# Optimization experiments

Hardware: AMD Instinct MI355X
Metric: run time of the kernel (lower is better)

## Reference

```python
import jax, jax.numpy as jnp
import numpy as np

B, T, I, H, O = 64, 2048, 128, 256, 128
K1 = 1
K2 = 1


def setup_inputs() -> dict:
    key = jax.random.key(0)
    ks = jax.random.split(key, 8)
    M = H - K1 + 1
    return {
        "x": jax.random.normal(ks[0], (B, T, I), jnp.float32),
        "W_in": jax.random.normal(ks[1], (H, I), jnp.float32) / np.sqrt(I).astype(np.float32),
        "b_in": jax.random.normal(ks[2], (H,), jnp.float32) * 0.01,
        "W_out": jax.random.normal(ks[3], (O, H), jnp.float32) / np.sqrt(H).astype(np.float32),
        "b_out": jax.random.normal(ks[4], (O,), jnp.float32) * 0.01,
        # padded Householder vectors: row i uses its first K+i entries (masked in reference)
        # uniform in [0.5, 1.5] keeps u.u well away from 0 (avoids 2/<u,u> blowup)
        "u_raw": jax.random.uniform(ks[5], (M, H), jnp.float32, 0.5, 1.5),
        "sigmas": jnp.ones((H,), jnp.float32),
        "v_raw": jax.random.uniform(ks[6], (M, H), jnp.float32, 0.5, 1.5),
    }


def _householder_chain(hats):
    # U <- H_last @ ... @ H_0, H_i = I - 2/<u,u> u u^T, applied as rank-1 updates
    Hdim = hats.shape[1]
    def step(Umat, u):
        beta = 2.0 / jnp.dot(u, u)
        return Umat - beta * jnp.outer(u, u @ Umat), None
    U, _ = jax.lax.scan(step, jnp.eye(Hdim, dtype=hats.dtype), hats)
    return U


def reference(x, W_in, b_in, W_out, b_out, u_raw, sigmas, v_raw):
    Hdim = sigmas.shape[0]
    Mu = u_raw.shape[0]
    Mv = v_raw.shape[0]
    # row i of u_hats has entries in cols [0, K1+i), then flipped along cols
    mask_u = jnp.arange(Hdim)[None, :] < (K1 + jnp.arange(Mu))[:, None]
    u_hats = jnp.flip(jnp.where(mask_u, u_raw, 0.0), axis=1)
    mask_v = jnp.arange(Hdim)[None, :] < (K2 + jnp.arange(Mv))[:, None]
    v_hats = jnp.flip(jnp.where(mask_v, v_raw, 0.0), axis=(0, 1))  # torch.flip dims=[0,1]
    U = _householder_chain(u_hats)
    V = _householder_chain(v_hats)
    W = (U * sigmas[None, :]) @ V  # U @ diag(sigmas) @ V
    # precompute input projection for all timesteps: [T, B, H]
    xproj = jnp.einsum('bti,hi->tbh', x, W_in) + b_in
    h0 = jnp.zeros((x.shape[0], Hdim), x.dtype)
    def cell(h, xp):
        h = jnp.tanh(xp + h @ W.T)
        return h, h @ W_out.T + b_out
    _, out = jax.lax.scan(cell, h0, xproj)  # out: [T, B, O]
    return jnp.transpose(out, (1, 0, 2))
```

## Files before the change

### kernel.cpp

```cpp
#include <hip/hip_runtime.h>
#include <hip/hip_bf16.h>
#include <hip/hip_fp16.h>

#define BB 64
#define TT 2048
#define II 128
#define HH 256
#define OO 128
#define RCH 8

typedef _Float16 f16x2 __attribute__((ext_vector_type(2)));
typedef _Float16 f16x8 __attribute__((ext_vector_type(8)));
typedef float f32x4 __attribute__((ext_vector_type(4)));

#if __has_builtin(__builtin_amdgcn_fdot2)
__device__ __forceinline__ float fdot2(f16x2 a, f16x2 b, float c) {
    return __builtin_amdgcn_fdot2(a, b, c, false);
}
#else
__device__ __forceinline__ float fdot2(f16x2 a, f16x2 b, float c) {
    return fmaf((float)a.x, (float)b.x, fmaf((float)a.y, (float)b.y, c));
}
#endif

__device__ __forceinline__ f16x2 u2h(unsigned int u) { return __builtin_bit_cast(f16x2, u); }
__device__ __forceinline__ unsigned int packf16(float a, float b) {
    return __builtin_bit_cast(unsigned int, f16x2{(_Float16)a, (_Float16)b});
}

__device__ __forceinline__ float tanh_fast(float x) {
    float xc = fminf(fmaxf(x, -9.0f), 9.0f);
    float e = __expf(2.0f * xc);
    return (e - 1.0f) * __fdividef(1.0f, e + 1.0f);
}

__global__ __launch_bounds__(64) void prep_kernel(
    const float* __restrict__ u_raw, const float* __restrict__ v_raw,
    float* __restrict__ u_eff, float* __restrict__ v_eff,
    float* __restrict__ beta_u, float* __restrict__ beta_v)
{
    const int row = blockIdx.x;
    const int lane = threadIdx.x;
    const bool isU = row < HH;
    const int i = isU ? row : row - HH;
    const float* src = isU ? (u_raw + (size_t)i * HH) : (v_raw + (size_t)(HH - 1 - i) * HH);
    float* dst = (isU ? u_eff : v_eff) + (size_t)i * HH;
    const int lo = isU ? (HH - 1 - i) : i;
    float ss = 0.0f;
    for (int c = lane; c < HH; c += 64) {
        float vv = (c >= lo) ? src[HH - 1 - c] : 0.0f;
        dst[c] = vv;
        ss += vv * vv;
    }
    for (int m = 1; m < 64; m <<= 1) ss += __shfl_xor(ss, m, 64);
    if (lane == 0) (isU ? beta_u : beta_v)[i] = 2.0f / ss;
}

__global__ __launch_bounds__(256) void hh_kernel(
    const float* __restrict__ u_eff, const float* __restrict__ v_eff,
    const float* __restrict__ beta_u, const float* __restrict__ beta_v,
    float* __restrict__ Ucol, float* __restrict__ Vrow)
{
    const int wid = blockIdx.x * 4 + (threadIdx.x >> 6);
    const int lane = threadIdx.x & 63;
    const bool isU = wid < HH;
    const int j = isU ? wid : wid - HH;
    const float* eff = isU ? u_eff : v_eff;
    const float* beta = isU ? beta_u : beta_v;

    float cr0 = (j == 4 * lane + 0) ? 1.0f : 0.0f;
    float cr1 = (j == 4 * lane + 1) ? 1.0f : 0.0f;
    float cr2 = (j == 4 * lane + 2) ? 1.0f : 0.0f;
    float cr3 = (j == 4 * lane + 3) ? 1.0f : 0.0f;

    const int i0 = isU ? (HH - 1 - j) : 0;
    for (int i = i0; i < HH; ++i) {
        const float4 v4 = *(const float4*)(eff + (size_t)i * HH + lane * 4);
        float d = v4.x * cr0 + v4.y * cr1 + v4.z * cr2 + v4.w * cr3;
        for (int m = 1; m < 64; m <<= 1) d += __shfl_xor(d, m, 64);
        const float t = beta[i] * d;
        cr0 = fmaf(-t, v4.x, cr0);
        cr1 = fmaf(-t, v4.y, cr1);
        cr2 = fmaf(-t, v4.z, cr2);
        cr3 = fmaf(-t, v4.w, cr3);
    }
    if (isU) {
        *(float4*)(Ucol + (size_t)j * HH + lane * 4) = make_float4(cr0, cr1, cr2, cr3);
    } else {
        Vrow[(size_t)(4 * lane + 0) * HH + j] = cr0;
        Vrow[(size_t)(4 * lane + 1) * HH + j] = cr1;
        Vrow[(size_t)(4 * lane + 2) * HH + j] = cr2;
        Vrow[(size_t)(4 * lane + 3) * HH + j] = cr3;
    }
}

__global__ __launch_bounds__(256) void w_kernel(
    const float* __restrict__ Ucol, const float* __restrict__ Vrow,
    const float* __restrict__ sig, float* __restrict__ Wm)
{
    const int r = blockIdx.x;
    const int c = threadIdx.x;
    float acc = 0.0f;
    #pragma unroll 4
    for (int k = 0; k < HH; ++k) {
        acc = fmaf(Ucol[(size_t)k * HH + r] * sig[k], Vrow[(size_t)k * HH + c], acc);
    }
    Wm[(size_t)r * HH + c] = acc;
}

__device__ __forceinline__ void stage16(_Float16* dst, const float* src) {
    #pragma unroll
    for (int i = 0; i < 4; ++i) {
        float4 f = ((const float4*)src)[i];
        ((f16x2*)dst)[2 * i + 0] = f16x2{(_Float16)f.x, (_Float16)f.y};
        ((f16x2*)dst)[2 * i + 1] = f16x2{(_Float16)f.z, (_Float16)f.w};
    }
}
__device__ __forceinline__ void stage16(_Float16* dst, const __half* src) {
    ((uint4*)dst)[0] = ((const uint4*)src)[0];
    ((uint4*)dst)[1] = ((const uint4*)src)[1];
}
__device__ __forceinline__ void storeC(float* p, float v) { *p = v; }
__device__ __forceinline__ void storeC(__half* p, float v) { *p = __float2half_rn(v); }

template <typename AT, typename OT>
__global__ __launch_bounds__(256) void gemm_mfma(
    const AT* __restrict__ A, const float* __restrict__ Bm,
    const float* __restrict__ bias, OT* __restrict__ C,
    int M, int N, int K)
{
    __shared__ _Float16 As[128][40];
    __shared__ _Float16 Bs[64][40];
    const int tid = threadIdx.x;
    const int m0 = blockIdx.x * 128;
    const int n0 = blockIdx.y * 64;
    const int lane = tid & 63;
    const int w = tid >> 6;
    const int lo = lane & 15;
    const int qd = lane >> 4;
    const int mh = w >> 1;
    const int nh = w & 1;
    const int srow = tid >> 1;
    const int shalf = tid & 1;

    f32x4 acc[4][2] = {};
    for (int k0 = 0; k0 < K; k0 += 32) {
        stage16(&As[srow][shalf * 16], A + (size_t)(m0 + srow) * K + k0 + shalf * 16);
        if (tid < 128)
            stage16(&Bs[srow][shalf * 16], Bm + (size_t)(n0 + srow) * K + k0 + shalf * 16);
        __syncthreads();
        f16x8 af[4], bf[2];
        #pragma unroll
        for (int mt = 0; mt < 4; ++mt)
            af[mt] = *(const f16x8*)&As[64 * mh + 16 * mt + lo][qd * 8];
        #pragma unroll
        for (int nt = 0; nt < 2; ++nt)
            bf[nt] = *(const f16x8*)&Bs[32 * nh + 16 * nt + lo][qd * 8];
        #pragma unroll
        for (int mt = 0; mt < 4; ++mt)
            #pragma unroll
            for (int nt = 0; nt < 2; ++nt)
                acc[mt][nt] = __builtin_amdgcn_mfma_f32_16x16x32_f16(
                    af[mt], bf[nt], acc[mt][nt], 0, 0, 0);
        __syncthreads();
    }
    #pragma unroll
    for (int nt = 0; nt < 2; ++nt) {
        const int n = n0 + 32 * nh + 16 * nt + lo;
        const float bv = bias[n];
        #pragma unroll
        for (int mt = 0; mt < 4; ++mt) {
            const int m = m0 + 64 * mh + 16 * mt + 4 * qd;
            #pragma unroll
            for (int r = 0; r < 4; ++r)
                storeC(C + (size_t)(m + r) * N + n, acc[mt][nt][r] + bv);
        }
    }
}

__global__ __launch_bounds__(512) void recur_kernel(
    const float* __restrict__ Wm,
    const __half* __restrict__ xp,
    __half* __restrict__ hall)
{
    const int b = blockIdx.x;
    const int tid = threadIdx.x;
    const int l = tid & 63;
    const int q = tid >> 6;

    __shared__ float ps[8][HH];
    __shared__ unsigned int hbits[2][HH / 2];

    f16x2 w2[4][16];
    #pragma unroll
    for (int r = 0; r < 4; ++r) {
        const float* Wp = Wm + (size_t)(4 * l + r) * HH + q * 32;
        #pragma unroll
        for (int c4 = 0; c4 < 8; ++c4) {
            float4 f = *(const float4*)(Wp + c4 * 4);
            w2[r][c4 * 2 + 0] = f16x2{(_Float16)f.x, (_Float16)f.y};
            w2[r][c4 * 2 + 1] = f16x2{(_Float16)f.z, (_Float16)f.w};
        }
    }
    if (tid < HH / 2) hbits[0][tid] = 0u;
    __syncthreads();

    const unsigned int* xpw = (const unsigned int*)(xp + (size_t)b * TT * HH);
    unsigned int* hw = (unsigned int*)(hall + (size_t)b * TT * HH);

    unsigned int xpcur[RCH], xpnxt[RCH], hst[RCH];
    if (tid < 128) {
        #pragma unroll
        for (int s = 0; s < RCH; ++s) xpcur[s] = xpw[(size_t)s * 128 + tid];
    }

    const int nch = TT / RCH;
    for (int c = 0; c < nch; ++c) {
        #pragma unroll
        for (int s = 0; s < RCH; ++s) {
            const int p = s & 1;
            if (s == 0 && tid < 128 && c + 1 < nch) {
                const unsigned int* xn = xpw + (size_t)(c + 1) * RCH * 128 + tid;
                #pragma unroll
                for (int s2 = 0; s2 < RCH; ++s2) xpnxt[s2] = xn[(size_t)s2 * 128];
            }
            uint4 ha = *(const uint4*)&hbits[p][q * 16 + 0];
            uint4 hc = *(const uint4*)&hbits[p][q * 16 + 4];
            uint4 hd = *(const uint4*)&hbits[p][q * 16 + 8];
            uint4 he = *(const uint4*)&hbits[p][q * 16 + 12];
            f16x2 hv[16] = {
                u2h(ha.x), u2h(ha.y), u2h(ha.z), u2h(ha.w),
                u2h(hc.x), u2h(hc.y), u2h(hc.z), u2h(hc.w),
                u2h(hd.x), u2h(hd.y), u2h(hd.z), u2h(hd.w),
                u2h(he.x), u2h(he.y), u2h(he.z), u2h(he.w)};
            float a0 = 0.f, a1 = 0.f, a2 = 0.f, a3 = 0.f;
            #pragma unroll
            for (int cc = 0; cc < 16; ++cc) {
                a0 = fdot2(w2[0][cc], hv[cc], a0);
                a1 = fdot2(w2[1][cc], hv[cc], a1);
                a2 = fdot2(w2[2][cc], hv[cc], a2);
                a3 = fdot2(w2[3][cc], hv[cc], a3);
            }
            *(float4*)(&ps[q][4 * l]) = make_float4(a0, a1, a2, a3);
            __syncthreads();

            if (tid < 128) {
                float sx = 0.f, sy = 0.f;
                #pragma unroll
                for (int qq = 0; qq < 8; ++qq) {
                    float2 v = *(const float2*)&ps[qq][2 * tid];
                    sx += v.x; sy += v.y;
                }
                f16x2 xv = u2h(xpcur[s]);
                float h0 = tanh_fast(sx + (float)xv.x);
                float h1 = tanh_fast(sy + (float)xv.y);
                unsigned int hb2 = packf16(h0, h1);
                hbits[p ^ 1][tid] = hb2;
                hst[s] = hb2;
            }
            __syncthreads();
        }
        if (tid < 128) {
            unsigned int* hwc = hw + (size_t)c * RCH * 128 + tid;
            #pragma unroll
            for (int s = 0; s < RCH; ++s) hwc[(size_t)s * 128] = hst[s];
            #pragma unroll
            for (int s = 0; s < RCH; ++s) xpcur[s] = xpnxt[s];
        }
    }
}

extern "C" void kernel_launch(void* const* d_in, const int* in_sizes, int n_in,
                              void* d_out, int out_size, void* d_ws, size_t ws_size,
                              hipStream_t stream) {
    const float* x     = (const float*)d_in[0];
    const float* W_in  = (const float*)d_in[1];
    const float* b_in  = (const float*)d_in[2];
    const float* W_out = (const float*)d_in[3];
    const float* b_out = (const float*)d_in[4];
    const float* u_raw = (const float*)d_in[5];
    const float* sig   = (const float*)d_in[6];
    const float* v_raw = (const float*)d_in[7];
    float* out = (float*)d_out;

    char* ws = (char*)d_ws;
    size_t off = 0;
    auto alloc = [&](size_t bytes) -> void* {
        void* p = (void*)(ws + off);
        off += (bytes + 255) & ~((size_t)255);
        return p;
    };
    float* u_eff  = (float*)alloc((size_t)HH * HH * 4);
    float* v_eff  = (float*)alloc((size_t)HH * HH * 4);
    float* beta_u = (float*)alloc((size_t)HH * 4);
    float* beta_v = (float*)alloc((size_t)HH * 4);
    float* Ucol   = (float*)alloc((size_t)HH * HH * 4);
    float* Vrow   = (float*)alloc((size_t)HH * HH * 4);
    float* Wm     = (float*)alloc((size_t)HH * HH * 4);
    __half* xpbuf = (__half*)alloc((size_t)BB * TT * HH * 2);
    __half* hall  = (__half*)alloc((size_t)BB * TT * HH * 2);
    (void)ws_size; (void)in_sizes; (void)n_in; (void)out_size;

    prep_kernel<<<2 * HH, 64, 0, stream>>>(u_raw, v_raw, u_eff, v_eff, beta_u, beta_v);
    hh_kernel<<<(2 * HH) / 4, 256, 0, stream>>>(u_eff, v_eff, beta_u, beta_v, Ucol, Vrow);
    w_kernel<<<HH, HH, 0, stream>>>(Ucol, Vrow, sig, Wm);
    gemm_mfma<float, __half>
        <<<dim3((BB * TT) / 128, HH / 64), 256, 0, stream>>>(x, W_in, b_in, xpbuf, BB * TT, HH, II);
    recur_kernel<<<BB, 512, 0, stream>>>(Wm, xpbuf, hall);
    gemm_mfma<__half, float>
        <<<dim3((BB * TT) / 128, OO / 64), 256, 0, stream>>>(hall, W_out, b_out, out, BB * TT, OO, HH);
}
```

Measured before the change: 1.501 ms.

## Restructure recurrence to one barrier per step via row-split warps and shuffle reduction

Each thread now owns one W row half (128 columns) in registers, and the two halves are combined with a cross-lane shuffle. This replaces the shared-memory partial-sum buffer and its second __syncthreads per timestep. A custom barrier waits only on LDS counters, so the global xp prefetch loads are not drained at every step. The costs are 64 f16x2 weight registers per thread, broadcast LDS reads of the full h vector, and scalar f16 xp loads per thread.

```diff
diff --git a/kernel.cpp b/kernel.cpp
--- a/kernel.cpp
+++ b/kernel.cpp
@@ -32,6 +32,13 @@
     float xc = fminf(fmaxf(x, -9.0f), 9.0f);
     float e = __expf(2.0f * xc);
     return (e - 1.0f) * __fdividef(1.0f, e + 1.0f);
+}
+
+__device__ __forceinline__ void step_barrier() {
+    __builtin_amdgcn_sched_barrier(0);
+    asm volatile("s_waitcnt lgkmcnt(0)" ::: "memory");
+    __builtin_amdgcn_s_barrier();
+    __builtin_amdgcn_sched_barrier(0);
 }
 
 __global__ __launch_bounds__(64) void prep_kernel(
@@ -187,86 +194,71 @@
     const int tid = threadIdx.x;
     const int l = tid & 63;
     const int q = tid >> 6;
-
-    __shared__ float ps[8][HH];
-    __shared__ unsigned int hbits[2][HH / 2];
-
-    f16x2 w2[4][16];
+    const int lr = l & 31;
+    const int kh = l >> 5;
+
+    __shared__ __align__(16) unsigned int hbuf[2][HH / 2];
+
+    const int row = 32 * q + lr;
+    f16x2 w2[64];
+    {
+        const float* Wp = Wm + (size_t)row * HH + 128 * kh;
+        #pragma unroll
+        for (int c4 = 0; c4 < 32; ++c4) {
+            float4 f = *(const float4*)(Wp + 4 * c4);
+            w2[2 * c4 + 0] = f16x2{(_Float16)f.x, (_Float16)f.y};
+            w2[2 * c4 + 1] = f16x2{(_Float16)f.z, (_Float16)f.w};
+        }
+    }
+    if (tid < HH) ((unsigned int*)hbuf)[tid] = 0u;
+    __syncthreads();
+
+    const _Float16* xph = (const _Float16*)xp + (size_t)b * TT * HH + row;
+    unsigned int* hw = (unsigned int*)(hall + (size_t)b * TT * HH) + 16 * q + (lr >> 1);
+    const bool wr = (l < 32) && ((l & 1) == 0);
+
+    _Float16 xpc[RCH], xpn[RCH];
+    unsigned int hst[RCH];
     #pragma unroll
-    for (int r = 0; r < 4; ++r) {
-        const float* Wp = Wm + (size_t)(4 * l + r) * HH + q * 32;
-        #pragma unroll
-        for (int c4 = 0; c4 < 8; ++c4) {
-            float4 f = *(const float4*)(Wp + c4 * 4);
-            w2[r][c4 * 2 + 0] = f16x2{(_Float16)f.x, (_Float16)f.y};
-            w2[r][c4 * 2 + 1] = f16x2{(_Float16)f.z, (_Float16)f.w};
-        }
-    }
-    if (tid < HH / 2) hbits[0][tid] = 0u;
-    __syncthreads();
-
-    const unsigned int* xpw = (const unsigned int*)(xp + (size_t)b * TT * HH);
-    unsigned int* hw = (unsigned int*)(hall + (size_t)b * TT * HH);
-
-    unsigned int xpcur[RCH], xpnxt[RCH], hst[RCH];
-    if (tid < 128) {
-        #pragma unroll
-        for (int s = 0; s < RCH; ++s) xpcur[s] = xpw[(size_t)s * 128 + tid];
-    }
-
+    for (int s = 0; s < RCH; ++s) xpc[s] = xph[(size_t)s * HH];
+
+    int p = 0;
     const int nch = TT / RCH;
     for (int c = 0; c < nch; ++c) {
+        if (c + 1 < nch) {
+            const _Float16* xn = xph + (size_t)(c + 1) * RCH * HH;
+            #pragma unroll
+            for (int s = 0; s < RCH; ++s) xpn[s] = xn[(size_t)s * HH];
+        }
         #pragma unroll
         for (int s = 0; s < RCH; ++s) {
-            const int p = s & 1;
-            if (s == 0 && tid < 128 && c + 1 < nch) {
-                const unsigned int* xn = xpw + (size_t)(c + 1) * RCH * 128 + tid;
-                #pragma unroll
-                for (int s2 = 0; s2 < RCH; ++s2) xpnxt[s2] = xn[(size_t)s2 * 128];
+            const uint4* hb = (const uint4*)(&hbuf[p][0]) + kh * 16;
+            float a0 = 0.f, a1 = 0.f, a2 = 0.f, a3 = 0.f;
+            #pragma unroll
+            for (int g = 0; g < 16; ++g) {
+                uint4 h4 = hb[g];
+                a0 = fdot2(w2[4 * g + 0], u2h(h4.x), a0);
+                a1 = fdot2(w2[4 * g + 1], u2h(h4.y), a1);
+                a2 = fdot2(w2[4 * g + 2], u2h(h4.z), a2);
+                a3 = fdot2(w2[4 * g + 3], u2h(h4.w), a3);
             }
-            uint4 ha = *(const uint4*)&hbits[p][q * 16 + 0];
-            uint4 hc = *(const uint4*)&hbits[p][q * 16 + 4];
-            uint4 hd = *(const uint4*)&hbits[p][q * 16 + 8];
-            uint4 he = *(const uint4*)&hbits[p][q * 16 + 12];
-            f16x2 hv[16] = {
-                u2h(ha.x), u2h(ha.y), u2h(ha.z), u2h(ha.w),
-                u2h(hc.x), u2h(hc.y), u2h(hc.z), u2h(hc.w),
-                u2h(hd.x), u2h(hd.y), u2h(hd.z), u2h(hd.w),
-                u2h(he.x), u2h(he.y), u2h(he.z), u2h(he.w)};
-            float a0 = 0.f, a1 = 0.f, a2 = 0.f, a3 = 0.f;
-            #pragma unroll
-            for (int cc = 0; cc < 16; ++cc) {
-                a0 = fdot2(w2[0][cc], hv[cc], a0);
-                a1 = fdot2(w2[1][cc], hv[cc], a1);
-                a2 = fdot2(w2[2][cc], hv[cc], a2);
-                a3 = fdot2(w2[3][cc], hv[cc], a3);
-            }
-            *(float4*)(&ps[q][4 * l]) = make_float4(a0, a1, a2, a3);
-            __syncthreads();
-
-            if (tid < 128) {
-                float sx = 0.f, sy = 0.f;
-                #pragma unroll
-                for (int qq = 0; qq < 8; ++qq) {
-                    float2 v = *(const float2*)&ps[qq][2 * tid];
-                    sx += v.x; sy += v.y;
-                }
-                f16x2 xv = u2h(xpcur[s]);
-                float h0 = tanh_fast(sx + (float)xv.x);
-                float h1 = tanh_fast(sy + (float)xv.y);
-                unsigned int hb2 = packf16(h0, h1);
-                hbits[p ^ 1][tid] = hb2;
-                hst[s] = hb2;
-            }
-            __syncthreads();
-        }
-        if (tid < 128) {
-            unsigned int* hwc = hw + (size_t)c * RCH * 128 + tid;
+            float part = (a0 + a1) + (a2 + a3);
+            float tot = part + __shfl_xor(part, 32, 64);
+            float hval = tanh_fast(tot + (float)xpc[s]);
+            float hot = __shfl_xor(hval, 1, 64);
+            unsigned int pk = packf16(hval, hot);
+            hst[s] = pk;
+            if (wr) hbuf[p ^ 1][16 * q + (lr >> 1)] = pk;
+            step_barrier();
+            p ^= 1;
+        }
+        if (wr) {
+            unsigned int* hwc = hw + (size_t)c * RCH * 128;
             #pragma unroll
             for (int s = 0; s < RCH; ++s) hwc[(size_t)s * 128] = hst[s];
-            #pragma unroll
-            for (int s = 0; s < RCH; ++s) xpcur[s] = xpnxt[s];
-        }
+        }
+        #pragma unroll
+        for (int s = 0; s < RCH; ++s) xpc[s] = xpn[s];
     }
 }
 
```

New measurement: 1.550 ms. 1.03x slower.

## Process two batch rows per recurrence block and use lightweight LDS barriers

Applied to the files above, without the earlier changes.

The recurrence kernel now handles two batch sequences per 512-thread block, reusing the register-resident fp16 W for both. That doubles the dot-product work per step while keeping the same number of barriers, and halves the grid to 32 blocks. The __syncthreads calls are replaced by a custom barrier that waits only on LDS counters, with sched_barrier fences around it. The costs are fewer active CUs, higher register pressure, and more arithmetic on the serial critical path of each block.

```diff
diff --git a/kernel.cpp b/kernel.cpp
--- a/kernel.cpp
+++ b/kernel.cpp
@@ -32,6 +32,13 @@
     float xc = fminf(fmaxf(x, -9.0f), 9.0f);
     float e = __expf(2.0f * xc);
     return (e - 1.0f) * __fdividef(1.0f, e + 1.0f);
+}
+
+__device__ __forceinline__ void step_barrier() {
+    __builtin_amdgcn_sched_barrier(0);
+    asm volatile("s_waitcnt lgkmcnt(0)" ::: "memory");
+    __builtin_amdgcn_s_barrier();
+    __builtin_amdgcn_sched_barrier(0);
 }
 
 __global__ __launch_bounds__(64) void prep_kernel(
@@ -183,13 +190,13 @@
     const __half* __restrict__ xp,
     __half* __restrict__ hall)
 {
-    const int b = blockIdx.x;
+    const int b0 = blockIdx.x * 2;
     const int tid = threadIdx.x;
     const int l = tid & 63;
     const int q = tid >> 6;
 
-    __shared__ float ps[8][HH];
-    __shared__ unsigned int hbits[2][HH / 2];
+    __shared__ float ps[2][8][HH];
+    __shared__ unsigned int hbits[2][2][HH / 2];
 
     f16x2 w2[4][16];
     #pragma unroll
@@ -202,16 +209,18 @@
             w2[r][c4 * 2 + 1] = f16x2{(_Float16)f.z, (_Float16)f.w};
         }
     }
-    if (tid < HH / 2) hbits[0][tid] = 0u;
+    if (tid < 256) hbits[tid >> 7][0][tid & 127] = 0u;
     __syncthreads();
 
-    const unsigned int* xpw = (const unsigned int*)(xp + (size_t)b * TT * HH);
-    unsigned int* hw = (unsigned int*)(hall + (size_t)b * TT * HH);
+    const int bb = tid >> 7;
+    const int t2 = tid & 127;
+    const unsigned int* xpw = (const unsigned int*)(xp + (size_t)(b0 + bb) * TT * HH);
+    unsigned int* hw = (unsigned int*)(hall + (size_t)(b0 + bb) * TT * HH);
 
     unsigned int xpcur[RCH], xpnxt[RCH], hst[RCH];
-    if (tid < 128) {
-        #pragma unroll
-        for (int s = 0; s < RCH; ++s) xpcur[s] = xpw[(size_t)s * 128 + tid];
+    if (tid < 256) {
+        #pragma unroll
+        for (int s = 0; s < RCH; ++s) xpcur[s] = xpw[(size_t)s * 128 + t2];
     }
 
     const int nch = TT / RCH;
@@ -219,49 +228,60 @@
         #pragma unroll
         for (int s = 0; s < RCH; ++s) {
             const int p = s & 1;
-            if (s == 0 && tid < 128 && c + 1 < nch) {
-                const unsigned int* xn = xpw + (size_t)(c + 1) * RCH * 128 + tid;
+            if (s == 0 && tid < 256 && c + 1 < nch) {
+                const unsigned int* xn = xpw + (size_t)(c + 1) * RCH * 128 + t2;
                 #pragma unroll
                 for (int s2 = 0; s2 < RCH; ++s2) xpnxt[s2] = xn[(size_t)s2 * 128];
             }
-            uint4 ha = *(const uint4*)&hbits[p][q * 16 + 0];
-            uint4 hc = *(const uint4*)&hbits[p][q * 16 + 4];
-            uint4 hd = *(const uint4*)&hbits[p][q * 16 + 8];
-            uint4 he = *(const uint4*)&hbits[p][q * 16 + 12];
-            f16x2 hv[16] = {
-                u2h(ha.x), u2h(ha.y), u2h(ha.z), u2h(ha.w),
-                u2h(hc.x), u2h(hc.y), u2h(hc.z), u2h(hc.w),
-                u2h(hd.x), u2h(hd.y), u2h(hd.z), u2h(hd.w),
-                u2h(he.x), u2h(he.y), u2h(he.z), u2h(he.w)};
+            const uint4* hbA = (const uint4*)&hbits[0][p][q * 16];
+            const uint4* hbB = (const uint4*)&hbits[1][p][q * 16];
+            uint4 A0 = hbA[0], A1 = hbA[1], A2 = hbA[2], A3 = hbA[3];
+            uint4 B0 = hbB[0], B1 = hbB[1], B2 = hbB[2], B3 = hbB[3];
+            f16x2 hA[16] = {
+                u2h(A0.x), u2h(A0.y), u2h(A0.z), u2h(A0.w),
+                u2h(A1.x), u2h(A1.y), u2h(A1.z), u2h(A1.w),
+                u2h(A2.x), u2h(A2.y), u2h(A2.z), u2h(A2.w),
+                u2h(A3.x), u2h(A3.y), u2h(A3.z), u2h(A3.w)};
+            f16x2 hB[16] = {
+                u2h(B0.x), u2h(B0.y), u2h(B0.z), u2h(B0.w),
+                u2h(B1.x), u2h(B1.y), u2h(B1.z), u2h(B1.w),
+                u2h(B2.x), u2h(B2.y), u2h(B2.z), u2h(B2.w),
+                u2h(B3.x), u2h(B3.y), u2h(B3.z), u2h(B3.w)};
             float a0 = 0.f, a1 = 0.f, a2 = 0.f, a3 = 0.f;
+            float b0a = 0.f, b1a = 0.f, b2a = 0.f, b3a = 0.f;
             #pragma unroll
             for (int cc = 0; cc < 16; ++cc) {
-                a0 = fdot2(w2[0][cc], hv[cc], a0);
-                a1 = fdot2(w2[1][cc], hv[cc], a1);
-                a2 = fdot2(w2[2][cc], hv[cc], a2);
-                a3 = fdot2(w2[3][cc], hv[cc], a3);
+                a0 = fdot2(w2[0][cc], hA[cc], a0);
+                a1 = fdot2(w2[1][cc], hA[cc], a1);
+                a2 = fdot2(w2[2][cc], hA[cc], a2);
+                a3 = fdot2(w2[3][cc], hA[cc], a3);
+                b0a = fdot2(w2[0][cc], hB[cc], b0a);
+                b1a = fdot2(w2[1][cc], hB[cc], b1a);
+                b2a = fdot2(w2[2][cc], hB[cc], b2a);
+                b3a = fdot2(w2[3][cc], hB[cc], b3a);
             }
-            *(float4*)(&ps[q][4 * l]) = make_float4(a0, a1, a2, a3);
-            __syncthreads();
-
-            if (tid < 128) {
+            *(float4*)(&ps[0][q][4 * l]) = make_float4(a0, a1, a2, a3);
+            *(float4*)(&ps[1][q][4 * l]) = make_float4(b0a, b1a, b2a, b3a);
+            step_barrier();
+
+            if (tid < 256) {
                 float sx = 0.f, sy = 0.f;
                 #pragma unroll
                 for (int qq = 0; qq < 8; ++qq) {
-                    float2 v = *(const float2*)&ps[qq][2 * tid];
+                    float2 v = *(const float2*)&ps[bb][qq][2 * t2];
                     sx += v.x; sy += v.y;
                 }
                 f16x2 xv = u2h(xpcur[s]);
                 float h0 = tanh_fast(sx + (float)xv.x);
                 float h1 = tanh_fast(sy + (float)xv.y);
                 unsigned int hb2 = packf16(h0, h1);
-                hbits[p ^ 1][tid] = hb2;
+                hbits[bb][p ^ 1][t2] = hb2;
                 hst[s] = hb2;
             }
-            __syncthreads();
+            step_barrier();
         }
-        if (tid < 128) {
-            unsigned int* hwc = hw + (size_t)c * RCH * 128 + tid;
+        if (tid < 256) {
+            unsigned int* hwc = hw + (size_t)c * RCH * 128 + t2;
             #pragma unroll
             for (int s = 0; s < RCH; ++s) hwc[(size_t)s * 128] = hst[s];
             #pragma unroll
@@ -306,7 +326,7 @@
     w_kernel<<<HH, HH, 0, stream>>>(Ucol, Vrow, sig, Wm);
     gemm_mfma<float, __half>
         <<<dim3((BB * TT) / 128, HH / 64), 256, 0, stream>>>(x, W_in, b_in, xpbuf, BB * TT, HH, II);
-    recur_kernel<<<BB, 512, 0, stream>>>(Wm, xpbuf, hall);
+    recur_kernel<<<BB / 2, 512, 0, stream>>>(Wm, xpbuf, hall);
     gemm_mfma<__half, float>
         <<<dim3((BB * TT) / 128, OO / 64), 256, 0, stream>>>(hall, W_out, b_out, out, BB * TT, OO, HH);
 }
```

Result: slower. 2.118 ms (+41.1%).
